# Kernel tuning notes

Hardware: AMD Instinct MI355X
Metric: run time of the kernel (lower is better)

The kernel has to match this reference:

```python
import jax, jax.numpy as jnp
import numpy as np

N = 1048576  # number of frequency sampling points
K = 64       # number of cascaded SVF sections


def setup_inputs() -> dict:
    key = jax.random.key(0)
    ks = jax.random.split(key, 7)
    return {
        "x_real": jax.random.normal(ks[0], (N,), dtype=jnp.float32),
        "x_imag": jax.random.normal(ks[1], (N,), dtype=jnp.float32),
        "f":   jax.random.normal(ks[2], (1, K), dtype=jnp.float32),
        "R":   jax.random.normal(ks[3], (1, K), dtype=jnp.float32),
        "mLP": jax.random.normal(ks[4], (1, K), dtype=jnp.float32),
        "mBP": jax.random.normal(ks[5], (1, K), dtype=jnp.float32),
        "mHP": jax.random.normal(ks[6], (1, K), dtype=jnp.float32),
    }


def reference(x_real, x_imag, f, R, mLP, mBP, mHP):
    # x: complex sampling points (z on / near the unit circle)
    x = jax.lax.complex(x_real, x_imag)  # [N] complex64
    f, R, mLP, mBP, mHP = f[0], R[0], mLP[0], mBP[0], mHP[0]  # [K]
    f2 = f * f
    # biquad coefficients, [3, K]
    beta = jnp.stack([
        f2 * mLP + f * mBP + mHP,
        2.0 * f2 * mLP - 2.0 * mHP,
        f2 * mLP - f * mBP + mHP,
    ])
    alpha = jnp.stack([
        f2 + 2.0 * R * f + 1.0,
        2.0 * f2 - 2.0,
        f2 - 2.0 * R * f + 1.0,
    ])
    # X = [x^0, x^-1, x^-2], [N, 3] complex
    xinv = 1.0 / x
    X = jnp.stack([jnp.ones_like(x), xinv, xinv * xinv], axis=1)
    num = X @ beta.astype(X.dtype)    # [N, K]
    den = X @ alpha.astype(X.dtype)   # [N, K]
    # original initializes H = 1 + 1j then multiplies all K sections
    H = (1.0 + 1.0j) * jnp.prod(num / den, axis=1)  # [N]
    return H
```

## Files before the change

### kernel.cpp

```cpp
#include <hip/hip_runtime.h>


#define NSEC  64
#define NHEX  8
#define DEG   16
#define NCF   34
#define BLOCK 256
#define MPT   2

__global__ __launch_bounds__(64) void svf_coef_v13(
    const float* __restrict__ f_g,  const float* __restrict__ R_g,
    const float* __restrict__ lp_g, const float* __restrict__ bp_g,
    const float* __restrict__ hp_g,
    float* __restrict__ coef)
{
    const int t = threadIdx.x;
    if (t >= NHEX) return;

    double pn[DEG + 1], pd[DEG + 1];
    #pragma unroll
    for (int j = 0; j <= DEG; ++j) { pn[j] = 0.0; pd[j] = 0.0; }
    pn[0] = 1.0; pd[0] = 1.0;

    #pragma unroll
    for (int s = 0; s < 8; ++s) {
        const int k = 8 * t + s;
        const double fk = (double)f_g[k],  Rk = (double)R_g[k];
        const double lp = (double)lp_g[k], bp = (double)bp_g[k], hp = (double)hp_g[k];
        const double f2 = fk * fk, fbp = fk * bp, flp = f2 * lp, rf2 = 2.0 * Rk * fk;
        const double bb0 = flp - fbp + hp;
        const double bb1 = 2.0 * flp - 2.0 * hp;
        const double bb2 = flp + fbp + hp;
        const double aa0 = f2 - rf2 + 1.0;
        const double aa1 = 2.0 * f2 - 2.0;
        const double aa2 = f2 + rf2 + 1.0;

        double nn[DEG + 1], nd[DEG + 1];
        #pragma unroll
        for (int j = 0; j <= DEG; ++j) { nn[j] = 0.0; nd[j] = 0.0; }
        #pragma unroll
        for (int i = 0; i <= DEG - 2; ++i) {
            nn[i]     += pn[i] * bb0;
            nn[i + 1] += pn[i] * bb1;
            nn[i + 2] += pn[i] * bb2;
            nd[i]     += pd[i] * aa0;
            nd[i + 1] += pd[i] * aa1;
            nd[i + 2] += pd[i] * aa2;
        }
        #pragma unroll
        for (int j = 0; j <= DEG; ++j) { pn[j] = nn[j]; pd[j] = nd[j]; }
    }

    double mx = 0.0;
    #pragma unroll
    for (int j = 0; j <= DEG; ++j) mx = fmax(mx, fabs(pd[j]));
    const double sc = (mx > 0.0) ? ldexp(1.0, -ilogb(mx)) : 1.0;

    float* cp = coef + t * NCF;
    #pragma unroll
    for (int j = 0; j <= DEG; ++j) {
        cp[j]          = (float)(pn[j] * sc);
        cp[17 + j]     = (float)(pd[j] * sc);
    }
}

#define CSQ(dr_, di_, ar_, ai_)                                   \
    dr_ = fmaf((ar_), (ar_), -((ai_) * (ai_)));                   \
    di_ = 2.0f * ((ar_) * (ai_));
#define CMUL(dr_, di_, ar_, ai_, br_, bi_)                        \
    dr_ = fmaf((ar_), (br_), -((ai_) * (bi_)));                   \
    di_ = fmaf((ar_), (bi_),  ((ai_) * (br_)));

__global__ __launch_bounds__(BLOCK, 4) void svf_f32_v13(
    const float* __restrict__ xr_g, const float* __restrict__ xi_g,
    const float* __restrict__ coef,
    float* __restrict__ out, int n, long long cap_floats)
{
    const int t = threadIdx.x;
    const long long base = (long long)(blockIdx.x * BLOCK + t) * MPT;

    float Xr[16][MPT], Xi[16][MPT];
    float Hr[MPT], Hi[MPT];

    if (base + MPT <= (long long)n) {
        const float2 a = *reinterpret_cast<const float2*>(xr_g + base);
        const float2 b = *reinterpret_cast<const float2*>(xi_g + base);
        Xr[0][0] = a.x; Xr[0][1] = a.y;
        Xi[0][0] = b.x; Xi[0][1] = b.y;
    } else {
        for (int m = 0; m < MPT; ++m) {
            const long long idx = base + m;
            const bool ok = idx < (long long)n;
            Xr[0][m] = ok ? xr_g[idx] : 1.0f;
            Xi[0][m] = ok ? xi_g[idx] : 0.0f;
        }
    }

    #pragma unroll
    for (int m = 0; m < MPT; ++m) {
        CSQ (Xr[1][m],  Xi[1][m],  Xr[0][m], Xi[0][m]);
        CMUL(Xr[2][m],  Xi[2][m],  Xr[1][m], Xi[1][m], Xr[0][m], Xi[0][m]);
        CSQ (Xr[3][m],  Xi[3][m],  Xr[1][m], Xi[1][m]);
        CMUL(Xr[4][m],  Xi[4][m],  Xr[3][m], Xi[3][m], Xr[0][m], Xi[0][m]);
        CSQ (Xr[5][m],  Xi[5][m],  Xr[2][m], Xi[2][m]);
        CMUL(Xr[6][m],  Xi[6][m],  Xr[3][m], Xi[3][m], Xr[2][m], Xi[2][m]);
        CSQ (Xr[7][m],  Xi[7][m],  Xr[3][m], Xi[3][m]);
        CMUL(Xr[8][m],  Xi[8][m],  Xr[7][m], Xi[7][m], Xr[0][m], Xi[0][m]);
        CSQ (Xr[9][m],  Xi[9][m],  Xr[4][m], Xi[4][m]);
        CMUL(Xr[10][m], Xi[10][m], Xr[7][m], Xi[7][m], Xr[2][m], Xi[2][m]);
        CSQ (Xr[11][m], Xi[11][m], Xr[5][m], Xi[5][m]);
        CMUL(Xr[12][m], Xi[12][m], Xr[7][m], Xi[7][m], Xr[4][m], Xi[4][m]);
        CSQ (Xr[13][m], Xi[13][m], Xr[6][m], Xi[6][m]);
        CMUL(Xr[14][m], Xi[14][m], Xr[7][m], Xi[7][m], Xr[6][m], Xi[6][m]);
        CSQ (Xr[15][m], Xi[15][m], Xr[7][m], Xi[7][m]);
        Hr[m] = 1.0f;
        Hi[m] = 1.0f;
    }

    #pragma unroll
    for (int p = 0; p < NHEX; ++p) {
        const float* cp = coef + p * NCF;
        float cn[17], cd[17];
        #pragma unroll
        for (int j = 0; j < 17; ++j) { cn[j] = cp[j]; cd[j] = cp[17 + j]; }

        #pragma unroll
        for (int m = 0; m < MPT; ++m) {
            float nr = cn[0], ni = 0.0f, dr = cd[0], di = 0.0f;
            #pragma unroll
            for (int q = 1; q <= 16; ++q) {
                nr = fmaf(cn[q], Xr[q - 1][m], nr);
                ni = fmaf(cn[q], Xi[q - 1][m], ni);
                dr = fmaf(cd[q], Xr[q - 1][m], dr);
                di = fmaf(cd[q], Xi[q - 1][m], di);
            }
            const float dd  = fmaf(dr, dr, di * di);
            const float inv = __builtin_amdgcn_rcpf(dd);
            const float tr  = fmaf(nr, dr,   ni * di);
            const float ti  = fmaf(ni, dr, -(nr * di));
            const float rr  = tr * inv;
            const float ri  = ti * inv;
            const float hr = fmaf(Hr[m], rr, -(Hi[m] * ri));
            const float hi = fmaf(Hr[m], ri,   Hi[m] * rr);
            Hr[m] = hr; Hi[m] = hi;
        }
    }

    const long long imag_off = (long long)n;
    if (base + MPT <= (long long)n && 2LL * (long long)n <= cap_floats) {
        float2 vr, vi;
        vr.x = Hr[0]; vr.y = Hr[1];
        vi.x = Hi[0]; vi.y = Hi[1];
        *reinterpret_cast<float2*>(out + base)            = vr;
        *reinterpret_cast<float2*>(out + imag_off + base) = vi;
    } else {
        for (int m = 0; m < MPT; ++m) {
            const long long idx = base + m;
            if (idx < (long long)n) {
                if (idx + 1 <= cap_floats) out[idx] = Hr[m];
                const long long oi = imag_off + idx;
                if (oi + 1 <= cap_floats) out[oi] = Hi[m];
            }
        }
    }
}

extern "C" void kernel_launch(void* const* d_in, const int* in_sizes, int n_in,
                              void* d_out, int out_size, void* d_ws, size_t ws_size,
                              hipStream_t stream) {
    const float* xr = (const float*)d_in[0];
    const float* xi = (const float*)d_in[1];
    const float* f  = (const float*)d_in[2];
    const float* R  = (const float*)d_in[3];
    const float* lp = (const float*)d_in[4];
    const float* bp = (const float*)d_in[5];
    const float* hp = (const float*)d_in[6];
    float* out = (float*)d_out;
    float* coef = (float*)d_ws;

    const int n = in_sizes[0];
    long long cap = (long long)out_size;
    if (cap > 2LL * (long long)n) cap = 2LL * (long long)n;

    svf_coef_v13<<<1, 64, 0, stream>>>(f, R, lp, bp, hp, coef);
    const int grid = (n + BLOCK * MPT - 1) / (BLOCK * MPT);
    svf_f32_v13<<<grid, BLOCK, 0, stream>>>(xr, xi, coef, out, n, cap);
}
```

Baseline: 83.69 us.

## Regroup cascade into sixteen degree-8 polynomial pairs, one point per thread

The coefficient kernel now merges 4 sections per group into degree-8 numerator/denominator polynomials (16 groups) instead of 8 sections into degree-16 (8 groups). The main kernel needs only powers x..x^8, processes one point per thread instead of two, and requests higher occupancy in its launch bounds. This cuts power computation and register pressure. The cost is twice as many complex divisions and running-product multiplies per point, and less reuse of each coefficient load. Lower-degree polynomials are also likely better conditioned in float32.

```diff
diff --git a/kernel.cpp b/kernel.cpp
--- a/kernel.cpp
+++ b/kernel.cpp
@@ -2,20 +2,19 @@
 
 
 #define NSEC  64
-#define NHEX  8
-#define DEG   16
-#define NCF   34
+#define NOCT  16
+#define DEG   8
+#define NCF   18
 #define BLOCK 256
-#define MPT   2
 
-__global__ __launch_bounds__(64) void svf_coef_v13(
+__global__ __launch_bounds__(64) void svf_coef_v14(
     const float* __restrict__ f_g,  const float* __restrict__ R_g,
     const float* __restrict__ lp_g, const float* __restrict__ bp_g,
     const float* __restrict__ hp_g,
     float* __restrict__ coef)
 {
     const int t = threadIdx.x;
-    if (t >= NHEX) return;
+    if (t >= NOCT) return;
 
     double pn[DEG + 1], pd[DEG + 1];
     #pragma unroll
@@ -23,8 +22,8 @@
     pn[0] = 1.0; pd[0] = 1.0;
 
     #pragma unroll
-    for (int s = 0; s < 8; ++s) {
-        const int k = 8 * t + s;
+    for (int s = 0; s < 4; ++s) {
+        const int k = 4 * t + s;
         const double fk = (double)f_g[k],  Rk = (double)R_g[k];
         const double lp = (double)lp_g[k], bp = (double)bp_g[k], hp = (double)hp_g[k];
         const double f2 = fk * fk, fbp = fk * bp, flp = f2 * lp, rf2 = 2.0 * Rk * fk;
@@ -59,8 +58,8 @@
     float* cp = coef + t * NCF;
     #pragma unroll
     for (int j = 0; j <= DEG; ++j) {
-        cp[j]          = (float)(pn[j] * sc);
-        cp[17 + j]     = (float)(pd[j] * sc);
+        cp[j]           = (float)(pn[j] * sc);
+        cp[DEG + 1 + j] = (float)(pd[j] * sc);
     }
 }
 
@@ -71,97 +70,59 @@
     dr_ = fmaf((ar_), (br_), -((ai_) * (bi_)));                   \
     di_ = fmaf((ar_), (bi_),  ((ai_) * (br_)));
 
-__global__ __launch_bounds__(BLOCK, 4) void svf_f32_v13(
+__global__ __launch_bounds__(BLOCK, 8) void svf_f32_v14(
     const float* __restrict__ xr_g, const float* __restrict__ xi_g,
     const float* __restrict__ coef,
     float* __restrict__ out, int n, long long cap_floats)
 {
-    const int t = threadIdx.x;
-    const long long base = (long long)(blockIdx.x * BLOCK + t) * MPT;
+    const long long idx = (long long)blockIdx.x * BLOCK + threadIdx.x;
+    const bool ok = idx < (long long)n;
 
-    float Xr[16][MPT], Xi[16][MPT];
-    float Hr[MPT], Hi[MPT];
+    const float x1r = ok ? xr_g[idx] : 1.0f;
+    const float x1i = ok ? xi_g[idx] : 0.0f;
 
-    if (base + MPT <= (long long)n) {
-        const float2 a = *reinterpret_cast<const float2*>(xr_g + base);
-        const float2 b = *reinterpret_cast<const float2*>(xi_g + base);
-        Xr[0][0] = a.x; Xr[0][1] = a.y;
-        Xi[0][0] = b.x; Xi[0][1] = b.y;
-    } else {
-        for (int m = 0; m < MPT; ++m) {
-            const long long idx = base + m;
-            const bool ok = idx < (long long)n;
-            Xr[0][m] = ok ? xr_g[idx] : 1.0f;
-            Xi[0][m] = ok ? xi_g[idx] : 0.0f;
+    float Xr[8], Xi[8];
+    Xr[0] = x1r; Xi[0] = x1i;
+    CSQ (Xr[1], Xi[1], Xr[0], Xi[0]);
+    CMUL(Xr[2], Xi[2], Xr[1], Xi[1], Xr[0], Xi[0]);
+    CSQ (Xr[3], Xi[3], Xr[1], Xi[1]);
+    CMUL(Xr[4], Xi[4], Xr[3], Xi[3], Xr[0], Xi[0]);
+    CSQ (Xr[5], Xi[5], Xr[2], Xi[2]);
+    CMUL(Xr[6], Xi[6], Xr[3], Xi[3], Xr[2], Xi[2]);
+    CSQ (Xr[7], Xi[7], Xr[3], Xi[3]);
+
+    float Hr = 1.0f, Hi = 1.0f;
+
+    #pragma unroll
+    for (int p = 0; p < NOCT; ++p) {
+        const float* cp = coef + p * NCF;
+        float cn[9], cd[9];
+        #pragma unroll
+        for (int j = 0; j < 9; ++j) { cn[j] = cp[j]; cd[j] = cp[9 + j]; }
+
+        float nr = cn[0], ni = 0.0f, dr = cd[0], di = 0.0f;
+        #pragma unroll
+        for (int q = 1; q <= 8; ++q) {
+            nr = fmaf(cn[q], Xr[q - 1], nr);
+            ni = fmaf(cn[q], Xi[q - 1], ni);
+            dr = fmaf(cd[q], Xr[q - 1], dr);
+            di = fmaf(cd[q], Xi[q - 1], di);
         }
+        const float dd  = fmaf(dr, dr, di * di);
+        const float inv = __builtin_amdgcn_rcpf(dd);
+        const float tr  = fmaf(nr, dr,   ni * di);
+        const float ti  = fmaf(ni, dr, -(nr * di));
+        const float rr  = tr * inv;
+        const float ri  = ti * inv;
+        const float hr = fmaf(Hr, rr, -(Hi * ri));
+        const float hi = fmaf(Hr, ri,   Hi * rr);
+        Hr = hr; Hi = hi;
     }
 
-    #pragma unroll
-    for (int m = 0; m < MPT; ++m) {
-        CSQ (Xr[1][m],  Xi[1][m],  Xr[0][m], Xi[0][m]);
-        CMUL(Xr[2][m],  Xi[2][m],  Xr[1][m], Xi[1][m], Xr[0][m], Xi[0][m]);
-        CSQ (Xr[3][m],  Xi[3][m],  Xr[1][m], Xi[1][m]);
-        CMUL(Xr[4][m],  Xi[4][m],  Xr[3][m], Xi[3][m], Xr[0][m], Xi[0][m]);
-        CSQ (Xr[5][m],  Xi[5][m],  Xr[2][m], Xi[2][m]);
-        CMUL(Xr[6][m],  Xi[6][m],  Xr[3][m], Xi[3][m], Xr[2][m], Xi[2][m]);
-        CSQ (Xr[7][m],  Xi[7][m],  Xr[3][m], Xi[3][m]);
-        CMUL(Xr[8][m],  Xi[8][m],  Xr[7][m], Xi[7][m], Xr[0][m], Xi[0][m]);
-        CSQ (Xr[9][m],  Xi[9][m],  Xr[4][m], Xi[4][m]);
-        CMUL(Xr[10][m], Xi[10][m], Xr[7][m], Xi[7][m], Xr[2][m], Xi[2][m]);
-        CSQ (Xr[11][m], Xi[11][m], Xr[5][m], Xi[5][m]);
-        CMUL(Xr[12][m], Xi[12][m], Xr[7][m], Xi[7][m], Xr[4][m], Xi[4][m]);
-        CSQ (Xr[13][m], Xi[13][m], Xr[6][m], Xi[6][m]);
-        CMUL(Xr[14][m], Xi[14][m], Xr[7][m], Xi[7][m], Xr[6][m], Xi[6][m]);
-        CSQ (Xr[15][m], Xi[15][m], Xr[7][m], Xi[7][m]);
-        Hr[m] = 1.0f;
-        Hi[m] = 1.0f;
-    }
-
-    #pragma unroll
-    for (int p = 0; p < NHEX; ++p) {
-        const float* cp = coef + p * NCF;
-        float cn[17], cd[17];
-        #pragma unroll
-        for (int j = 0; j < 17; ++j) { cn[j] = cp[j]; cd[j] = cp[17 + j]; }
-
-        #pragma unroll
-        for (int m = 0; m < MPT; ++m) {
-            float nr = cn[0], ni = 0.0f, dr = cd[0], di = 0.0f;
-            #pragma unroll
-            for (int q = 1; q <= 16; ++q) {
-                nr = fmaf(cn[q], Xr[q - 1][m], nr);
-                ni = fmaf(cn[q], Xi[q - 1][m], ni);
-                dr = fmaf(cd[q], Xr[q - 1][m], dr);
-                di = fmaf(cd[q], Xi[q - 1][m], di);
-            }
-            const float dd  = fmaf(dr, dr, di * di);
-            const float inv = __builtin_amdgcn_rcpf(dd);
-            const float tr  = fmaf(nr, dr,   ni * di);
-            const float ti  = fmaf(ni, dr, -(nr * di));
-            const float rr  = tr * inv;
-            const float ri  = ti * inv;
-            const float hr = fmaf(Hr[m], rr, -(Hi[m] * ri));
-            const float hi = fmaf(Hr[m], ri,   Hi[m] * rr);
-            Hr[m] = hr; Hi[m] = hi;
-        }
-    }
-
-    const long long imag_off = (long long)n;
-    if (base + MPT <= (long long)n && 2LL * (long long)n <= cap_floats) {
-        float2 vr, vi;
-        vr.x = Hr[0]; vr.y = Hr[1];
-        vi.x = Hi[0]; vi.y = Hi[1];
-        *reinterpret_cast<float2*>(out + base)            = vr;
-        *reinterpret_cast<float2*>(out + imag_off + base) = vi;
-    } else {
-        for (int m = 0; m < MPT; ++m) {
-            const long long idx = base + m;
-            if (idx < (long long)n) {
-                if (idx + 1 <= cap_floats) out[idx] = Hr[m];
-                const long long oi = imag_off + idx;
-                if (oi + 1 <= cap_floats) out[oi] = Hi[m];
-            }
-        }
+    if (ok) {
+        if (idx + 1 <= cap_floats) out[idx] = Hr;
+        const long long oi = (long long)n + idx;
+        if (oi + 1 <= cap_floats) out[oi] = Hi;
     }
 }
 
@@ -182,7 +143,7 @@
     long long cap = (long long)out_size;
     if (cap > 2LL * (long long)n) cap = 2LL * (long long)n;
 
-    svf_coef_v13<<<1, 64, 0, stream>>>(f, R, lp, bp, hp, coef);
-    const int grid = (n + BLOCK * MPT - 1) / (BLOCK * MPT);
-    svf_f32_v13<<<grid, BLOCK, 0, stream>>>(xr, xi, coef, out, n, cap);
+    svf_coef_v14<<<1, 64, 0, stream>>>(f, R, lp, bp, hp, coef);
+    const int grid = (n + BLOCK - 1) / BLOCK;
+    svf_f32_v14<<<grid, BLOCK, 0, stream>>>(xr, xi, coef, out, n, cap);
 }
```

Result: slower. 88.27 us (+5.5%).
